# Kernel optimization log

Hardware: AMD Instinct MI355X
Metric: run time of the kernel (lower is better)

The kernel has to match this reference:

```python
import jax, jax.numpy as jnp
from jax import lax
import numpy as np

B, S, I, H, L, D = 64, 1024, 512, 512, 2, 2  # batch, seq, input, hidden, layers, directions


def setup_inputs() -> dict:
    key = jax.random.key(0)
    ks = jax.random.split(key, 6)
    scale = 0.05  # keep gates out of saturation (torch code uses raw randn; scaled for numerics)
    return {
        "x": jax.random.normal(ks[0], (B, S, I), jnp.float32),
        "Wi": jax.random.normal(ks[1], (L, D, 3, I, H), jnp.float32) * scale,  # gates: [r, z, n]
        "Wh": jax.random.normal(ks[2], (L, D, 3, H, H), jnp.float32) * scale,
        "b": jax.random.normal(ks[3], (L, D, 3, H), jnp.float32) * scale,
        "fc_w": jax.random.normal(ks[4], (D * H, H), jnp.float32) * scale,
        "fc_b": jax.random.normal(ks[5], (H,), jnp.float32) * scale,
    }


def _run_layer(x_seq, wi, wh, bb):
    """One GRU layer, one direction. x_seq: [B,S,Hin]; wi/wh: [3,Hin,H]; bb: [3,H]."""
    batch = x_seq.shape[0]
    h_dim = wh.shape[-1]
    # Precompute all input projections (+biases) once: [S, 3, B, H]
    xs = jnp.einsum('bsi,gih->sgbh', x_seq, wi) + bb[None, :, None, :]

    def step(h, xg):
        r = jax.nn.sigmoid(xg[0] + h @ wh[0])
        z = jax.nn.sigmoid(xg[1] + h @ wh[1])
        n = jnp.tanh(xg[2] + r * (h @ wh[2]))
        h_next = (1.0 - z) * n + z * h
        return h_next, h_next

    h0 = jnp.zeros((batch, h_dim), x_seq.dtype)
    _, ys = lax.scan(step, h0, xs)  # ys: [S, B, H]
    return ys.transpose(1, 0, 2)  # [B, S, H]


def reference(x, Wi, Wh, b, fc_w, fc_b):
    n_layers = Wi.shape[0]
    # forward direction: stack layers, feed layer output as next layer input
    out_f = x
    for l in range(n_layers):
        out_f = _run_layer(out_f, Wi[l, 0], Wh[l, 0], b[l, 0])
    # backward direction: process time-reversed sequence, then flip back
    out_b = x[:, ::-1, :]
    for l in range(n_layers):
        out_b = _run_layer(out_b, Wi[l, 1], Wh[l, 1], b[l, 1])
    out_b = out_b[:, ::-1, :]
    outputs = jnp.concatenate([out_f, out_b], axis=2)  # [B, S, 2H]
    return outputs[:, -1, :] @ fc_w + fc_b  # [B, H]
```

## Files before the change

kernel.cpp:

```cpp
#include <hip/hip_runtime.h>
#include <cstdint>
#include <cmath>


typedef __attribute__((ext_vector_type(8))) short bf16x8;
typedef __attribute__((ext_vector_type(4))) float f32x4;
typedef __attribute__((ext_vector_type(4))) unsigned int u32x4;

#define DEV static __device__ __forceinline__

DEV unsigned short f2bf(float f) {
  union { float f; uint32_t u; } v; v.f = f;
  uint32_t u = v.u;
  return (unsigned short)((u + (((u >> 16) & 1u) + 0x7fffu)) >> 16);
}
DEV float bf2f(unsigned short h) {
  union { uint32_t u; float f; } v; v.u = ((uint32_t)h) << 16;
  return v.f;
}
DEV float fsig(float x)  { return 1.f / (1.f + __expf(-x)); }
DEV float ftanh(float x) { return 2.f / (1.f + __expf(-2.f * x)) - 1.f; }

static constexpr int Ss = 1024, Ii = 512;

static constexpr size_t WIMG_PER_LS = 131072;
static constexpr size_t OFF_WIMG = 0;
static constexpr size_t WIMG_BYTES = (size_t)64 * WIMG_PER_LS;
static constexpr size_t OFF_H1  = OFF_WIMG + WIMG_BYTES;
static constexpr size_t OFF_H2  = OFF_H1 + 524288;
static constexpr size_t OFF_FLG = OFF_H2 + 524288;
static constexpr size_t OFF_H2F = OFF_FLG + 4096;
static constexpr size_t OFF_HB1 = OFF_H2F + 131072;
static constexpr size_t OFF_HB2 = OFF_HB1 + 131072;
static constexpr size_t WS_NEED = OFF_HB2 + 131072;

__global__ __launch_bounds__(256) void prep_weights(const float* __restrict__ Wi,
                                                    const float* __restrict__ Wh,
                                                    unsigned short* __restrict__ img) {
  uint32_t idx = blockIdx.x * 256 + threadIdx.x;
  uint32_t ls = idx >> 16;
  uint32_t off = idx & 65535u;
  int l = (int)(ls >> 5), s = (int)(ls & 31);
  int m, g, cc, kg, kr;
  bool lo = off >= 49152u;
  if (!lo) {
    m = (int)(off / 24576u); uint32_t r = off % 24576u;
    kg = (int)(r / 384u); r %= 384u;
    int c = (int)(r >> 3); kr = (int)(r & 7u);
    g = c >> 4; cc = c & 15;
  } else {
    uint32_t o2 = off - 49152u;
    m = (int)(o2 >> 13); uint32_t r = o2 & 8191u;
    kg = (int)(r >> 7); r &= 127u;
    cc = (int)(r >> 3); kr = (int)(r & 7u);
    g = 2;
  }
  int h = s * 16 + cc, k = kg * 8 + kr;
  const float* W = m ? Wh : Wi;
  float v = W[((size_t)(l * 6 + g) * 512 + k) * 512 + h];
  unsigned short hv = f2bf(v);
  if (lo) hv = f2bf(v - bf2f(hv));
  img[(size_t)ls * 65536 + off] = hv;
}

__global__ __launch_bounds__(256) void init_state(uint32_t* __restrict__ hz,
                                                  int* __restrict__ flg) {
  int tid = blockIdx.x * 256 + threadIdx.x;
  if (tid < 262144) hz[tid] = 0u;
  if (tid < 1024) flg[tid] = ((tid & 15) == 0 && tid >= 512) ? 1 : 0;
}

#define MFMA(AA, BB, CC) CC = __builtin_amdgcn_mfma_f32_16x16x32_bf16(AA, BB, CC, 0, 0, 0)

DEV void wait_combined(int* flg, int tgtA, int tgtB, int lane) {
  int* p = flg + lane * 16;
  const int tgt = (lane < 32) ? tgtA : tgtB;
  int spins = 0;
  for (;;) {
    int v = __hip_atomic_load(p, __ATOMIC_RELAXED, __HIP_MEMORY_SCOPE_AGENT);
    if (__all(v >= tgt)) break;
    __builtin_amdgcn_s_sleep(4);
    if (++spins > (1 << 17)) {
      __hip_atomic_fetch_max(p, 0x40000000, __ATOMIC_RELAXED, __HIP_MEMORY_SCOPE_AGENT);
      break;
    }
  }
}

__global__ __launch_bounds__(256, 1) void gru_persistent(const float* __restrict__ x,
                                                         const float* __restrict__ bias,
                                                         unsigned char* __restrict__ ws) {
  __shared__ unsigned char lds[131072];
  const int tid = threadIdx.x, lane = tid & 63, wv = tid >> 6;
  const int bid = blockIdx.x;
  const int xcd = bid & 7;
  const int layer = xcd >> 2;
  const int slice = (xcd & 3) * 8 + (bid >> 3);
  const int l15 = lane & 15, q = lane >> 4;

  {
    const u32x4* src = (const u32x4*)(ws + OFF_WIMG + (size_t)(layer * 32 + slice) * WIMG_PER_LS);
    u32x4* dst = (u32x4*)lds;
    for (int i = tid; i < 8192; i += 256) dst[i] = src[i];
  }
  __syncthreads();

  bf16x8 hB[48];
#pragma unroll
  for (int kk = 0; kk < 16; ++kk) {
    const int kg = kk * 4 + q;
    const unsigned char* wb = lds + 49152 + (size_t)kg * 768 + (size_t)l15 * 16;
    hB[kk * 3 + 0] = *(const bf16x8*)(wb);
    hB[kk * 3 + 1] = *(const bf16x8*)(wb + 256);
    hB[kk * 3 + 2] = *(const bf16x8*)(wb + 512);
  }

  unsigned short* h1 = (unsigned short*)(ws + OFF_H1);
  unsigned short* h2 = (unsigned short*)(ws + OFF_H2);
  int* flg = (int*)(ws + OFF_FLG);
  float* h2f = (float*)(ws + OFF_H2F);

  const int colg = slice * 16 + l15;
  const int row0 = wv * 16 + q * 4;
  const float b0 = bias[(size_t)(layer * 6 + 0) * 512 + colg];
  const float b1 = bias[(size_t)(layer * 6 + 1) * 512 + colg];
  const float b2 = bias[(size_t)(layer * 6 + 2) * 512 + colg];

  int* myflag = flg + (layer * 32 + slice) * 16;
  f32x4 hprev{0.f, 0.f, 0.f, 0.f};

  if (layer == 0) {
    const float* xr0 = x + (size_t)(wv * 16 + l15) * Ss * Ii;
    for (int T = 1; T <= 1024; ++T) {
      f32x4 ax0{}, ax1{}, ax2{}, ah0{}, ah1{}, ah2{};
      const float* xr = xr0 + (size_t)(T - 1) * Ii;
#pragma unroll 4
      for (int kk = 0; kk < 16; ++kk) {
        const int kg = kk * 4 + q;
        f32x4 va = *(const f32x4*)(xr + kg * 8);
        f32x4 vb = *(const f32x4*)(xr + kg * 8 + 4);
        bf16x8 ahi, alo;
#pragma unroll
        for (int e = 0; e < 4; ++e) {
          unsigned short ha = f2bf(va[e]);
          ((unsigned short*)&ahi)[e] = ha;
          ((unsigned short*)&alo)[e] = f2bf(va[e] - bf2f(ha));
          unsigned short hb_ = f2bf(vb[e]);
          ((unsigned short*)&ahi)[e + 4] = hb_;
          ((unsigned short*)&alo)[e + 4] = f2bf(vb[e] - bf2f(hb_));
        }
        const unsigned char* wb = lds + (size_t)kg * 768 + (size_t)l15 * 16;
        bf16x8 q0 = *(const bf16x8*)(wb);
        bf16x8 q1 = *(const bf16x8*)(wb + 256);
        bf16x8 q2 = *(const bf16x8*)(wb + 512);
        bf16x8 ql = *(const bf16x8*)(lds + 98304 + (size_t)kg * 256 + (size_t)l15 * 16);
        MFMA(ahi, q0, ax0); MFMA(alo, q0, ax0);
        MFMA(ahi, q1, ax1); MFMA(alo, q1, ax1);
        MFMA(ahi, q2, ax2); MFMA(alo, q2, ax2);
        MFMA(ahi, ql, ax2);
      }
      if (wv == 0) {
        wait_combined(flg, T - 1, T - 3, lane);
        __builtin_amdgcn_fence(__ATOMIC_ACQUIRE, "agent");
      }
      __syncthreads();
      const unsigned short* hsrc = h1 + (size_t)((T - 1) & 3) * 65536 + (size_t)(wv * 16 + l15) * 512;
#pragma unroll
      for (int kk = 0; kk < 16; ++kk) {
        const int kg = kk * 4 + q;
        bf16x8 ahi = *(const bf16x8*)(hsrc + kg * 8);
        bf16x8 alo = *(const bf16x8*)(hsrc + 32768 + kg * 8);
        bf16x8 ql = *(const bf16x8*)(lds + 98304 + 16384 + (size_t)kg * 256 + (size_t)l15 * 16);
        MFMA(ahi, hB[kk * 3 + 0], ah0); MFMA(alo, hB[kk * 3 + 0], ah0);
        MFMA(ahi, hB[kk * 3 + 1], ah1); MFMA(alo, hB[kk * 3 + 1], ah1);
        MFMA(ahi, hB[kk * 3 + 2], ah2); MFMA(alo, hB[kk * 3 + 2], ah2);
        MFMA(ahi, ql, ah2);
      }
      unsigned short* hd = h1 + (size_t)(T & 3) * 65536;
#pragma unroll
      for (int e = 0; e < 4; ++e) {
        float rr = fsig(ax0[e] + ah0[e] + b0);
        float zz = fsig(ax1[e] + ah1[e] + b1);
        float nn = ftanh(ax2[e] + b2 + rr * ah2[e]);
        float hn = (1.f - zz) * nn + zz * hprev[e];
        hprev[e] = hn;
        unsigned short hi = f2bf(hn), lo = f2bf(hn - bf2f(hi));
        size_t o = (size_t)(row0 + e) * 512 + colg;
        hd[o] = hi; hd[o + 32768] = lo;
      }
      __syncthreads();
      if (tid == 0)
        __hip_atomic_fetch_max(myflag, T, __ATOMIC_RELEASE, __HIP_MEMORY_SCOPE_AGENT);
    }
  } else {
    for (int T = 2; T <= 1025; ++T) {
      if (wv == 0) {
        wait_combined(flg, T - 1, T - 1, lane);
        __builtin_amdgcn_fence(__ATOMIC_ACQUIRE, "agent");
      }
      __syncthreads();
      f32x4 ax0{}, ax1{}, ax2{}, ah0{}, ah1{}, ah2{};
      const unsigned short* hsrc = h2 + (size_t)((T - 2) & 3) * 65536 + (size_t)(wv * 16 + l15) * 512;
#pragma unroll
      for (int kk = 0; kk < 16; ++kk) {
        const int kg = kk * 4 + q;
        bf16x8 ahi = *(const bf16x8*)(hsrc + kg * 8);
        bf16x8 alo = *(const bf16x8*)(hsrc + 32768 + kg * 8);
        bf16x8 ql = *(const bf16x8*)(lds + 98304 + 16384 + (size_t)kg * 256 + (size_t)l15 * 16);
        MFMA(ahi, hB[kk * 3 + 0], ah0); MFMA(alo, hB[kk * 3 + 0], ah0);
        MFMA(ahi, hB[kk * 3 + 1], ah1); MFMA(alo, hB[kk * 3 + 1], ah1);
        MFMA(ahi, hB[kk * 3 + 2], ah2); MFMA(alo, hB[kk * 3 + 2], ah2);
        MFMA(ahi, ql, ah2);
      }
      const unsigned short* as = h1 + (size_t)((T - 1) & 3) * 65536 + (size_t)(wv * 16 + l15) * 512;
#pragma unroll 4
      for (int kk = 0; kk < 16; ++kk) {
        const int kg = kk * 4 + q;
        bf16x8 ahi = *(const bf16x8*)(as + kg * 8);
        bf16x8 alo = *(const bf16x8*)(as + 32768 + kg * 8);
        const unsigned char* wb = lds + (size_t)kg * 768 + (size_t)l15 * 16;
        bf16x8 q0 = *(const bf16x8*)(wb);
        bf16x8 q1 = *(const bf16x8*)(wb + 256);
        bf16x8 q2 = *(const bf16x8*)(wb + 512);
        bf16x8 ql = *(const bf16x8*)(lds + 98304 + (size_t)kg * 256 + (size_t)l15 * 16);
        MFMA(ahi, q0, ax0); MFMA(alo, q0, ax0);
        MFMA(ahi, q1, ax1); MFMA(alo, q1, ax1);
        MFMA(ahi, q2, ax2); MFMA(alo, q2, ax2);
        MFMA(ahi, ql, ax2);
      }
      unsigned short* hd = h2 + (size_t)((T - 1) & 3) * 65536;
#pragma unroll
      for (int e = 0; e < 4; ++e) {
        float rr = fsig(ax0[e] + ah0[e] + b0);
        float zz = fsig(ax1[e] + ah1[e] + b1);
        float nn = ftanh(ax2[e] + b2 + rr * ah2[e]);
        float hn = (1.f - zz) * nn + zz * hprev[e];
        hprev[e] = hn;
        unsigned short hi = f2bf(hn), lo = f2bf(hn - bf2f(hi));
        size_t o = (size_t)(row0 + e) * 512 + colg;
        hd[o] = hi; hd[o + 32768] = lo;
        if (T == 1025) h2f[o] = hn;
      }
      __syncthreads();
      if (tid == 0)
        __hip_atomic_fetch_max(myflag, T, __ATOMIC_RELEASE, __HIP_MEMORY_SCOPE_AGENT);
    }
  }
}

__global__ __launch_bounds__(256) void gru_bstep(const float* __restrict__ inp, long rstride,
                                                 const float* __restrict__ Wi,
                                                 const float* __restrict__ bias,
                                                 float* __restrict__ out) {
  __shared__ float a[8192];
  int tid = threadIdx.x;
  int bg = blockIdx.x >> 4, cg = blockIdx.x & 15;
  for (int j = 0; j < 32; ++j) {
    int idx = j * 256 + tid;
    int r = idx >> 9, k = idx & 511;
    a[idx] = inp[(size_t)(bg * 16 + r) * rstride + k];
  }
  __syncthreads();
  int col = cg * 32 + (tid & 31);
  int r0 = tid >> 5;
  float z0 = bias[512 + col], z1 = z0;
  float n0 = bias[1024 + col], n1 = n0;
  const float* W1 = Wi + (size_t)512 * 512;
  const float* W2 = Wi + (size_t)2 * 512 * 512;
  for (int k = 0; k < 512; ++k) {
    float wz = W1[(size_t)k * 512 + col];
    float wn = W2[(size_t)k * 512 + col];
    float a0 = a[r0 * 512 + k], a1 = a[(r0 + 8) * 512 + k];
    z0 += a0 * wz; z1 += a1 * wz;
    n0 += a0 * wn; n1 += a1 * wn;
  }
  float s0 = fsig(z0), s1 = fsig(z1);
  out[(size_t)(bg * 16 + r0) * 512 + col]     = (1.f - s0) * ftanh(n0);
  out[(size_t)(bg * 16 + r0 + 8) * 512 + col] = (1.f - s1) * ftanh(n1);
}

__global__ __launch_bounds__(256) void fc_kernel(const float* __restrict__ h2f,
                                                 const float* __restrict__ hb2,
                                                 const float* __restrict__ fcw,
                                                 const float* __restrict__ fcb,
                                                 float* __restrict__ out) {
  __shared__ float a[16384];
  int tid = threadIdx.x;
  int bg = blockIdx.x >> 4, cg = blockIdx.x & 15;
  for (int j = 0; j < 32; ++j) {
    int idx = j * 256 + tid;
    int r = idx >> 9, k = idx & 511;
    a[r * 1024 + k]       = h2f[(size_t)(bg * 16 + r) * 512 + k];
    a[r * 1024 + 512 + k] = hb2[(size_t)(bg * 16 + r) * 512 + k];
  }
  __syncthreads();
  int col = cg * 32 + (tid & 31);
  int r0 = tid >> 5;
  float s0 = fcb[col], s1 = fcb[col];
  for (int k = 0; k < 1024; ++k) {
    float wvv = fcw[(size_t)k * 512 + col];
    s0 += a[r0 * 1024 + k] * wvv;
    s1 += a[(r0 + 8) * 1024 + k] * wvv;
  }
  out[(size_t)(bg * 16 + r0) * 512 + col]     = s0;
  out[(size_t)(bg * 16 + r0 + 8) * 512 + col] = s1;
}

extern "C" void kernel_launch(void* const* d_in, const int* in_sizes, int n_in,
                              void* d_out, int out_size, void* d_ws, size_t ws_size,
                              hipStream_t stream) {
  const float* x   = (const float*)d_in[0];
  const float* Wi  = (const float*)d_in[1];
  const float* Wh  = (const float*)d_in[2];
  const float* b   = (const float*)d_in[3];
  const float* fcw = (const float*)d_in[4];
  const float* fcb = (const float*)d_in[5];
  float* out = (float*)d_out;
  unsigned char* ws = (unsigned char*)d_ws;
  if (ws_size < WS_NEED) return;

  prep_weights<<<16384, 256, 0, stream>>>(Wi, Wh, (unsigned short*)(ws + OFF_WIMG));
  init_state<<<1024, 256, 0, stream>>>((uint32_t*)(ws + OFF_H1), (int*)(ws + OFF_FLG));
  gru_persistent<<<64, 256, 0, stream>>>(x, b, ws);
  gru_bstep<<<64, 256, 0, stream>>>(x + (size_t)1023 * 512, (long)Ss * Ii,
                                    Wi + (size_t)3 * 512 * 512, b + 3 * 512,
                                    (float*)(ws + OFF_HB1));
  gru_bstep<<<64, 256, 0, stream>>>((const float*)(ws + OFF_HB1), 512L,
                                    Wi + (size_t)9 * 512 * 512, b + 9 * 512,
                                    (float*)(ws + OFF_HB2));
  fc_kernel<<<64, 256, 0, stream>>>((const float*)(ws + OFF_H2F), (const float*)(ws + OFF_HB2),
                                    fcw, fcb, out);
}
```

Baseline: 15.22 ms.

## Use cache-bypassing loads/stores for cross-block sync and pipeline h loads

Replaces the agent-scope atomic flag waits, acquire fences and release atomics with sc0 sc1 cache-coherent global loads and stores plus explicit vmcnt waits. The recurrent h operand loads become explicitly software-pipelined batches interleaved with MFMA groups. Layer 0's input projection for the next step is moved after the flag publish so it overlaps with waiting. This cuts synchronization latency on the serial recurrence critical path, but the correctness of the memory ordering now rests on hand-written inline asm. The spin timeout also drops to a short limit once it has fired.

Result: faster. 13.74 ms (-9.7%).

```diff
diff --git a/kernel.cpp b/kernel.cpp
--- a/kernel.cpp
+++ b/kernel.cpp
@@ -71,21 +71,105 @@
 }
 
 #define MFMA(AA, BB, CC) CC = __builtin_amdgcn_mfma_f32_16x16x32_bf16(AA, BB, CC, 0, 0, 0)
-
-DEV void wait_combined(int* flg, int tgtA, int tgtB, int lane) {
-  int* p = flg + lane * 16;
+#define SB0 __builtin_amdgcn_sched_barrier(0)
+#define VMWAIT0 asm volatile("s_waitcnt vmcnt(0)" ::: "memory")
+#define VMWAIT8 asm volatile("s_waitcnt vmcnt(8)" ::: "memory")
+#define LD16CP(dst, addr) \
+  asm volatile("global_load_dwordx4 %0, %1, off sc0 sc1" : "=&v"(dst) : "v"((const void*)(addr)))
+#define ST2CP(addr, val) \
+  asm volatile("global_store_short %0, %1, off sc0 sc1" :: "v"((void*)(addr)), "v"((uint32_t)(val)) : "memory")
+#define ST4CP(addr, val) \
+  asm volatile("global_store_dword %0, %1, off sc0 sc1" :: "v"((void*)(addr)), "v"(val) : "memory")
+
+DEV int pollcp(const int* p) {
+  int v;
+  asm volatile("global_load_dword %0, %1, off sc0 sc1\ns_waitcnt vmcnt(0)"
+               : "=v"(v) : "v"((const void*)p) : "memory");
+  return v;
+}
+
+DEV void wait_combined(int* flg, int tgtA, int tgtB, int lane, int& alive) {
+  const int* p = flg + lane * 16;
   const int tgt = (lane < 32) ? tgtA : tgtB;
+  const int lim = alive ? (1 << 17) : 64;
   int spins = 0;
   for (;;) {
-    int v = __hip_atomic_load(p, __ATOMIC_RELAXED, __HIP_MEMORY_SCOPE_AGENT);
+    int v = pollcp(p);
     if (__all(v >= tgt)) break;
-    __builtin_amdgcn_s_sleep(4);
-    if (++spins > (1 << 17)) {
-      __hip_atomic_fetch_max(p, 0x40000000, __ATOMIC_RELAXED, __HIP_MEMORY_SCOPE_AGENT);
-      break;
-    }
-  }
-}
+    __builtin_amdgcn_s_sleep(1);
+    if (++spins > lim) { alive = 0; break; }
+  }
+}
+
+#define ISSUE8(R, ABASE, BOFF)                                                 \
+  _Pragma("unroll")                                                            \
+  for (int j = 0; j < 4; ++j) {                                                \
+    LD16CP(R[2*j],   (ABASE) + (BOFF) + 64 * j);                               \
+    LD16CP(R[2*j+1], (ABASE) + (BOFF) + 64 * j + 65536);                       \
+  }
+#define MFB_REG(R, b, A0, A1, A2)                                              \
+  _Pragma("unroll")                                                            \
+  for (int j = 0; j < 4; ++j) {                                                \
+    const int kk = 4 * (b) + j;                                                \
+    const int kg = 16 * (b) + 4 * j + q;                                       \
+    bf16x8 ql = *(const bf16x8*)(lds + 98304 + 16384 + (size_t)kg * 256 + (size_t)l15 * 16); \
+    MFMA(R[2*j], hB[kk*3+0], A0); MFMA(R[2*j+1], hB[kk*3+0], A0);              \
+    MFMA(R[2*j], hB[kk*3+1], A1); MFMA(R[2*j+1], hB[kk*3+1], A1);              \
+    MFMA(R[2*j], hB[kk*3+2], A2); MFMA(R[2*j+1], hB[kk*3+2], A2);              \
+    MFMA(R[2*j], ql, A2);                                                      \
+  }
+#define MFB_LDSB(R, b, A0, A1, A2)                                             \
+  _Pragma("unroll")                                                            \
+  for (int j = 0; j < 4; ++j) {                                                \
+    const int kg = 16 * (b) + 4 * j + q;                                       \
+    const unsigned char* wb = lds + (size_t)kg * 768 + (size_t)l15 * 16;       \
+    bf16x8 q0 = *(const bf16x8*)(wb);                                          \
+    bf16x8 q1 = *(const bf16x8*)(wb + 256);                                    \
+    bf16x8 q2 = *(const bf16x8*)(wb + 512);                                    \
+    bf16x8 ql = *(const bf16x8*)(lds + 98304 + (size_t)kg * 256 + (size_t)l15 * 16); \
+    MFMA(R[2*j], q0, A0); MFMA(R[2*j+1], q0, A0);                              \
+    MFMA(R[2*j], q1, A1); MFMA(R[2*j+1], q1, A1);                              \
+    MFMA(R[2*j], q2, A2); MFMA(R[2*j+1], q2, A2);                              \
+    MFMA(R[2*j], ql, A2);                                                      \
+  }
+#define HGEMM(ABASE, MFB, A0, A1, A2)                                          \
+  {                                                                            \
+    bf16x8 fa[8], fb[8];                                                       \
+    SB0; ISSUE8(fa, ABASE, 0)  SB0; ISSUE8(fb, ABASE, 256) SB0;                \
+    VMWAIT8; SB0; MFB(fa, 0, A0, A1, A2) SB0;                                  \
+    ISSUE8(fa, ABASE, 512) SB0; VMWAIT8; SB0; MFB(fb, 1, A0, A1, A2) SB0;      \
+    ISSUE8(fb, ABASE, 768) SB0; VMWAIT8; SB0; MFB(fa, 2, A0, A1, A2) SB0;      \
+    VMWAIT0; SB0; MFB(fb, 3, A0, A1, A2) SB0;                                  \
+  }
+#define XGEMM(T0)                                                              \
+  {                                                                            \
+    const float* xr = xr0 + (size_t)(T0) * Ii;                                 \
+    _Pragma("unroll 4")                                                        \
+    for (int kk = 0; kk < 16; ++kk) {                                          \
+      const int kg = kk * 4 + q;                                               \
+      f32x4 va = *(const f32x4*)(xr + kg * 8);                                 \
+      f32x4 vb = *(const f32x4*)(xr + kg * 8 + 4);                             \
+      bf16x8 ahi, alo;                                                         \
+      _Pragma("unroll")                                                        \
+      for (int e = 0; e < 4; ++e) {                                            \
+        unsigned short ha = f2bf(va[e]);                                       \
+        ((unsigned short*)&ahi)[e] = ha;                                       \
+        ((unsigned short*)&alo)[e] = f2bf(va[e] - bf2f(ha));                   \
+        unsigned short hb_ = f2bf(vb[e]);                                      \
+        ((unsigned short*)&ahi)[e + 4] = hb_;                                  \
+        ((unsigned short*)&alo)[e + 4] = f2bf(vb[e] - bf2f(hb_));              \
+      }                                                                        \
+      const unsigned char* wb = lds + (size_t)kg * 768 + (size_t)l15 * 16;     \
+      bf16x8 q0 = *(const bf16x8*)(wb);                                        \
+      bf16x8 q1 = *(const bf16x8*)(wb + 256);                                  \
+      bf16x8 q2 = *(const bf16x8*)(wb + 512);                                  \
+      bf16x8 ql = *(const bf16x8*)(lds + 98304 + (size_t)kg * 256 + (size_t)l15 * 16); \
+      MFMA(ahi, q0, ax0); MFMA(alo, q0, ax0);                                  \
+      MFMA(ahi, q1, ax1); MFMA(alo, q1, ax1);                                  \
+      MFMA(ahi, q2, ax2); MFMA(alo, q2, ax2);                                  \
+      MFMA(ahi, ql, ax2);                                                      \
+    }                                                                          \
+  }
 
 __global__ __launch_bounds__(256, 1) void gru_persistent(const float* __restrict__ x,
                                                          const float* __restrict__ bias,
@@ -115,68 +199,33 @@
     hB[kk * 3 + 2] = *(const bf16x8*)(wb + 512);
   }
 
-  unsigned short* h1 = (unsigned short*)(ws + OFF_H1);
-  unsigned short* h2 = (unsigned short*)(ws + OFF_H2);
+  unsigned char* h1b = ws + OFF_H1;
+  unsigned char* h2b = ws + OFF_H2;
   int* flg = (int*)(ws + OFF_FLG);
   float* h2f = (float*)(ws + OFF_H2F);
 
   const int colg = slice * 16 + l15;
   const int row0 = wv * 16 + q * 4;
+  const int arow = wv * 16 + l15;
   const float b0 = bias[(size_t)(layer * 6 + 0) * 512 + colg];
   const float b1 = bias[(size_t)(layer * 6 + 1) * 512 + colg];
   const float b2 = bias[(size_t)(layer * 6 + 2) * 512 + colg];
 
   int* myflag = flg + (layer * 32 + slice) * 16;
   f32x4 hprev{0.f, 0.f, 0.f, 0.f};
+  int alive = 1;
 
   if (layer == 0) {
-    const float* xr0 = x + (size_t)(wv * 16 + l15) * Ss * Ii;
+    const float* xr0 = x + (size_t)arow * Ss * Ii;
+    f32x4 ax0{}, ax1{}, ax2{};
+    XGEMM(0)
     for (int T = 1; T <= 1024; ++T) {
-      f32x4 ax0{}, ax1{}, ax2{}, ah0{}, ah1{}, ah2{};
-      const float* xr = xr0 + (size_t)(T - 1) * Ii;
-#pragma unroll 4
-      for (int kk = 0; kk < 16; ++kk) {
-        const int kg = kk * 4 + q;
-        f32x4 va = *(const f32x4*)(xr + kg * 8);
-        f32x4 vb = *(const f32x4*)(xr + kg * 8 + 4);
-        bf16x8 ahi, alo;
-#pragma unroll
-        for (int e = 0; e < 4; ++e) {
-          unsigned short ha = f2bf(va[e]);
-          ((unsigned short*)&ahi)[e] = ha;
-          ((unsigned short*)&alo)[e] = f2bf(va[e] - bf2f(ha));
-          unsigned short hb_ = f2bf(vb[e]);
-          ((unsigned short*)&ahi)[e + 4] = hb_;
-          ((unsigned short*)&alo)[e + 4] = f2bf(vb[e] - bf2f(hb_));
-        }
-        const unsigned char* wb = lds + (size_t)kg * 768 + (size_t)l15 * 16;
-        bf16x8 q0 = *(const bf16x8*)(wb);
-        bf16x8 q1 = *(const bf16x8*)(wb + 256);
-        bf16x8 q2 = *(const bf16x8*)(wb + 512);
-        bf16x8 ql = *(const bf16x8*)(lds + 98304 + (size_t)kg * 256 + (size_t)l15 * 16);
-        MFMA(ahi, q0, ax0); MFMA(alo, q0, ax0);
-        MFMA(ahi, q1, ax1); MFMA(alo, q1, ax1);
-        MFMA(ahi, q2, ax2); MFMA(alo, q2, ax2);
-        MFMA(ahi, ql, ax2);
-      }
-      if (wv == 0) {
-        wait_combined(flg, T - 1, T - 3, lane);
-        __builtin_amdgcn_fence(__ATOMIC_ACQUIRE, "agent");
-      }
+      if (wv == 0) wait_combined(flg, T - 1, T - 3, lane, alive);
       __syncthreads();
-      const unsigned short* hsrc = h1 + (size_t)((T - 1) & 3) * 65536 + (size_t)(wv * 16 + l15) * 512;
-#pragma unroll
-      for (int kk = 0; kk < 16; ++kk) {
-        const int kg = kk * 4 + q;
-        bf16x8 ahi = *(const bf16x8*)(hsrc + kg * 8);
-        bf16x8 alo = *(const bf16x8*)(hsrc + 32768 + kg * 8);
-        bf16x8 ql = *(const bf16x8*)(lds + 98304 + 16384 + (size_t)kg * 256 + (size_t)l15 * 16);
-        MFMA(ahi, hB[kk * 3 + 0], ah0); MFMA(alo, hB[kk * 3 + 0], ah0);
-        MFMA(ahi, hB[kk * 3 + 1], ah1); MFMA(alo, hB[kk * 3 + 1], ah1);
-        MFMA(ahi, hB[kk * 3 + 2], ah2); MFMA(alo, hB[kk * 3 + 2], ah2);
-        MFMA(ahi, ql, ah2);
-      }
-      unsigned short* hd = h1 + (size_t)(T & 3) * 65536;
+      f32x4 ah0{}, ah1{}, ah2{};
+      const unsigned char* ab = h1b + (size_t)((T - 1) & 3) * 131072 + (size_t)arow * 1024 + (size_t)q * 16;
+      HGEMM(ab, MFB_REG, ah0, ah1, ah2)
+      unsigned char* hd = h1b + (size_t)(T & 3) * 131072;
 #pragma unroll
       for (int e = 0; e < 4; ++e) {
         float rr = fsig(ax0[e] + ah0[e] + b0);
@@ -185,50 +234,25 @@
         float hn = (1.f - zz) * nn + zz * hprev[e];
         hprev[e] = hn;
         unsigned short hi = f2bf(hn), lo = f2bf(hn - bf2f(hi));
-        size_t o = (size_t)(row0 + e) * 512 + colg;
-        hd[o] = hi; hd[o + 32768] = lo;
+        size_t ob = (size_t)(row0 + e) * 1024 + (size_t)colg * 2;
+        ST2CP(hd + ob, hi); ST2CP(hd + ob + 65536, lo);
       }
+      VMWAIT0;
       __syncthreads();
-      if (tid == 0)
-        __hip_atomic_fetch_max(myflag, T, __ATOMIC_RELEASE, __HIP_MEMORY_SCOPE_AGENT);
+      if (tid == 0) ST4CP(myflag, T);
+      ax0 = f32x4{}; ax1 = f32x4{}; ax2 = f32x4{};
+      if (T < 1024) XGEMM(T)
     }
   } else {
     for (int T = 2; T <= 1025; ++T) {
-      if (wv == 0) {
-        wait_combined(flg, T - 1, T - 1, lane);
-        __builtin_amdgcn_fence(__ATOMIC_ACQUIRE, "agent");
-      }
+      if (wv == 0) wait_combined(flg, T - 1, T - 1, lane, alive);
       __syncthreads();
       f32x4 ax0{}, ax1{}, ax2{}, ah0{}, ah1{}, ah2{};
-      const unsigned short* hsrc = h2 + (size_t)((T - 2) & 3) * 65536 + (size_t)(wv * 16 + l15) * 512;
-#pragma unroll
-      for (int kk = 0; kk < 16; ++kk) {
-        const int kg = kk * 4 + q;
-        bf16x8 ahi = *(const bf16x8*)(hsrc + kg * 8);
-        bf16x8 alo = *(const bf16x8*)(hsrc + 32768 + kg * 8);
-        bf16x8 ql = *(const bf16x8*)(lds + 98304 + 16384 + (size_t)kg * 256 + (size_t)l15 * 16);
-        MFMA(ahi, hB[kk * 3 + 0], ah0); MFMA(alo, hB[kk * 3 + 0], ah0);
-        MFMA(ahi, hB[kk * 3 + 1], ah1); MFMA(alo, hB[kk * 3 + 1], ah1);
-        MFMA(ahi, hB[kk * 3 + 2], ah2); MFMA(alo, hB[kk * 3 + 2], ah2);
-        MFMA(ahi, ql, ah2);
-      }
-      const unsigned short* as = h1 + (size_t)((T - 1) & 3) * 65536 + (size_t)(wv * 16 + l15) * 512;
-#pragma unroll 4
-      for (int kk = 0; kk < 16; ++kk) {
-        const int kg = kk * 4 + q;
-        bf16x8 ahi = *(const bf16x8*)(as + kg * 8);
-        bf16x8 alo = *(const bf16x8*)(as + 32768 + kg * 8);
-        const unsigned char* wb = lds + (size_t)kg * 768 + (size_t)l15 * 16;
-        bf16x8 q0 = *(const bf16x8*)(wb);
-        bf16x8 q1 = *(const bf16x8*)(wb + 256);
-        bf16x8 q2 = *(const bf16x8*)(wb + 512);
-        bf16x8 ql = *(const bf16x8*)(lds + 98304 + (size_t)kg * 256 + (size_t)l15 * 16);
-        MFMA(ahi, q0, ax0); MFMA(alo, q0, ax0);
-        MFMA(ahi, q1, ax1); MFMA(alo, q1, ax1);
-        MFMA(ahi, q2, ax2); MFMA(alo, q2, ax2);
-        MFMA(ahi, ql, ax2);
-      }
-      unsigned short* hd = h2 + (size_t)((T - 1) & 3) * 65536;
+      const unsigned char* ab2 = h2b + (size_t)((T - 2) & 3) * 131072 + (size_t)arow * 1024 + (size_t)q * 16;
+      HGEMM(ab2, MFB_REG, ah0, ah1, ah2)
+      const unsigned char* ab1 = h1b + (size_t)((T - 1) & 3) * 131072 + (size_t)arow * 1024 + (size_t)q * 16;
+      HGEMM(ab1, MFB_LDSB, ax0, ax1, ax2)
+      unsigned char* hd = h2b + (size_t)((T - 1) & 3) * 131072;
 #pragma unroll
       for (int e = 0; e < 4; ++e) {
         float rr = fsig(ax0[e] + ah0[e] + b0);
@@ -237,13 +261,13 @@
         float hn = (1.f - zz) * nn + zz * hprev[e];
         hprev[e] = hn;
         unsigned short hi = f2bf(hn), lo = f2bf(hn - bf2f(hi));
-        size_t o = (size_t)(row0 + e) * 512 + colg;
-        hd[o] = hi; hd[o + 32768] = lo;
-        if (T == 1025) h2f[o] = hn;
+        size_t ob = (size_t)(row0 + e) * 1024 + (size_t)colg * 2;
+        ST2CP(hd + ob, hi); ST2CP(hd + ob + 65536, lo);
+        if (T == 1025) h2f[(size_t)(row0 + e) * 512 + colg] = hn;
       }
+      VMWAIT0;
       __syncthreads();
-      if (tid == 0)
-        __hip_atomic_fetch_max(myflag, T, __ATOMIC_RELEASE, __HIP_MEMORY_SCOPE_AGENT);
+      if (tid == 0) ST4CP(myflag, T);
     }
   }
 }
```
